# Kernel optimization log

Measured on AMD Instinct MI355X. Metric: run time of the kernel, lower is better.

## Reference

```python
import jax, jax.numpy as jnp
import numpy as np

B, S, H, I, E, K = 8, 4096, 512, 2048, 8, 2

def setup_inputs() -> dict:
    key = jax.random.key(0)
    ks = jax.random.split(key, 7)
    sH = 1.0 / np.sqrt(H)
    sI = 1.0 / np.sqrt(I)
    return {
        "x": jax.random.normal(ks[0], (B, S, H), dtype=jnp.float32),
        "gate_w": jax.random.uniform(ks[1], (H, E), jnp.float32, -sH, sH),
        "gate_b": jnp.zeros((E,), jnp.float32),
        "w1": jax.random.uniform(ks[2], (E, H, I), jnp.float32, -sH, sH),
        "b1": jax.random.uniform(ks[3], (E, I), jnp.float32, -sH, sH),
        "w2": jax.random.uniform(ks[4], (E, I, H), jnp.float32, -sI, sI),
        "b2": jax.random.uniform(ks[5], (E, H), jnp.float32, -sI, sI),
    }

def reference(x, gate_w, gate_b, w1, b1, w2, b2):
    # Gating: softmax over experts, top-k, renormalize selected probs via softmax.
    gate_probs = jax.nn.softmax(x @ gate_w + gate_b, axis=-1)          # [B,S,E]
    top_v, top_i = jax.lax.top_k(gate_probs, K)                        # [B,S,K]
    top_w = jax.nn.softmax(top_v, axis=-1)                             # renormalized
    out = jnp.zeros_like(x)
    for e in range(E):  # small fixed expert count
        # combine weight per token for expert e (0 if not routed here)
        ce = jnp.sum(jnp.where(top_i == e, top_w, 0.0), axis=-1)       # [B,S]
        h = jax.nn.relu(jnp.einsum("bsh,hi->bsi", x, w1[e]) + b1[e])   # [B,S,I]
        ye = jnp.einsum("bsi,ih->bsh", h, w2[e]) + b2[e]               # [B,S,H]
        out = out + ce[..., None] * ye
    return out
```

## Files before the change

### kernel.cpp

```cpp
#include <hip/hip_runtime.h>
#include <hip/hip_bf16.h>
#include <cstdint>

#define T_TOK 32768
#define HD 512
#define ID 2048
#define NE 8
#define ROWS_PAD_MAX 66560

typedef __bf16 bf16x8 __attribute__((ext_vector_type(8)));
typedef float f32x4 __attribute__((ext_vector_type(4)));

__device__ __forceinline__ ushort f2bf(float f) {
  __hip_bfloat16 h = __float2bfloat16(f);
  return *reinterpret_cast<ushort*>(&h);
}

__device__ __forceinline__ void gload16(const ushort* g, ushort* l) {
  __builtin_amdgcn_global_load_lds((__attribute__((address_space(1))) void*)(void*)g,
                                   (__attribute__((address_space(3))) void*)(void*)l,
                                   16, 0, 0);
}

__global__ void k_zero(float4* out4, int n4, int* counts) {
  if (blockIdx.x == 0 && threadIdx.x < NE) counts[threadIdx.x] = 0;
  float4 z = make_float4(0.f, 0.f, 0.f, 0.f);
  for (int i = blockIdx.x * blockDim.x + threadIdx.x; i < n4; i += gridDim.x * blockDim.x)
    out4[i] = z;
}

__global__ void k_transpose(const float* __restrict__ in, ushort* __restrict__ out, int R, int C) {
  __shared__ float tile[32][33];
  int z = blockIdx.z;
  const float* src = in + (size_t)z * R * C;
  ushort* dst = out + (size_t)z * R * C;
  int c0 = blockIdx.x * 32, r0 = blockIdx.y * 32;
  int tx = threadIdx.x, ty = threadIdx.y;
#pragma unroll
  for (int i = 0; i < 32; i += 8)
    tile[ty + i][tx] = src[(size_t)(r0 + ty + i) * C + c0 + tx];
  __syncthreads();
#pragma unroll
  for (int i = 0; i < 32; i += 8)
    dst[(size_t)(c0 + ty + i) * R + r0 + tx] = f2bf(tile[tx][ty + i]);
}

__global__ __launch_bounds__(256) void k_cast_gate(const float* __restrict__ x,
                                                   const float* __restrict__ gw,
                                                   const float* __restrict__ gb,
                                                   ushort* __restrict__ xb,
                                                   uchar2* __restrict__ tope,
                                                   float2* __restrict__ tw) {
  int t = blockIdx.x * 4 + (threadIdx.x >> 6);
  int lane = threadIdx.x & 63;
  const float4* xr = (const float4*)(x + (size_t)t * HD);
  float4 v0 = xr[lane];
  float4 v1 = xr[lane + 64];
  ushort4 o0, o1;
  o0.x = f2bf(v0.x); o0.y = f2bf(v0.y); o0.z = f2bf(v0.z); o0.w = f2bf(v0.w);
  o1.x = f2bf(v1.x); o1.y = f2bf(v1.y); o1.z = f2bf(v1.z); o1.w = f2bf(v1.w);
  ushort4* xw = (ushort4*)(xb + (size_t)t * HD);
  xw[lane] = o0;
  xw[lane + 64] = o1;
  float xv[8] = {v0.x, v0.y, v0.z, v0.w, v1.x, v1.y, v1.z, v1.w};
  float p[8] = {0, 0, 0, 0, 0, 0, 0, 0};
  const float* g0 = gw + (size_t)lane * 4 * 8;
  const float* g1 = gw + (size_t)(256 + lane * 4) * 8;
#pragma unroll
  for (int j = 0; j < 4; ++j)
#pragma unroll
    for (int e = 0; e < 8; ++e) p[e] += xv[j] * g0[j * 8 + e];
#pragma unroll
  for (int j = 0; j < 4; ++j)
#pragma unroll
    for (int e = 0; e < 8; ++e) p[e] += xv[4 + j] * g1[j * 8 + e];
#pragma unroll
  for (int e = 0; e < 8; ++e) {
    float s = p[e];
    for (int off = 32; off; off >>= 1) s += __shfl_xor(s, off);
    p[e] = s + gb[e];
  }
  float mx = p[0];
#pragma unroll
  for (int e = 1; e < 8; ++e) mx = fmaxf(mx, p[e]);
  float Z = 0.f;
  float pr[8];
#pragma unroll
  for (int e = 0; e < 8; ++e) { pr[e] = expf(p[e] - mx); Z += pr[e]; }
  float invZ = 1.f / Z;
#pragma unroll
  for (int e = 0; e < 8; ++e) pr[e] *= invZ;
  float v1v = pr[0]; int i1 = 0;
#pragma unroll
  for (int e = 1; e < 8; ++e) { if (pr[e] > v1v) { v1v = pr[e]; i1 = e; } }
  float v2v = -1.f; int i2 = 0;
#pragma unroll
  for (int e = 0; e < 8; ++e) { if (e != i1 && pr[e] > v2v) { v2v = pr[e]; i2 = e; } }
  float c1 = 1.f / (1.f + expf(v2v - v1v));
  float c2 = 1.f - c1;
  if (lane == 0) {
    tope[t] = make_uchar2((unsigned char)i1, (unsigned char)i2);
    tw[t] = make_float2(c1, c2);
  }
}

__global__ __launch_bounds__(256) void k_route(const uchar2* __restrict__ tope,
                                               const float2* __restrict__ tw,
                                               int* __restrict__ rtok, float* __restrict__ rw,
                                               int* __restrict__ counts) {
  int t = blockIdx.x * 256 + threadIdx.x;
  int lane = threadIdx.x & 63;
  uchar2 ei = tope[t];
  float2 c = tw[t];
  unsigned long long below = (1ull << lane) - 1ull;
#pragma unroll
  for (int e = 0; e < NE; ++e) {
    bool sel = (ei.x == e) || (ei.y == e);
    unsigned long long mask = __ballot(sel);
    if (mask == 0ull) continue;
    int cnt = __popcll(mask);
    int base = 0;
    if (lane == 0) base = atomicAdd(&counts[e], cnt);
    base = __shfl(base, 0);
    if (sel) {
      int pos = base + __popcll(mask & below);
      rtok[e * T_TOK + pos] = t;
      rw[e * T_TOK + pos] = (ei.x == e) ? c.x : c.y;
    }
  }
}

__global__ void k_offsets(const int* __restrict__ counts, int* __restrict__ poff) {
  if (threadIdx.x == 0) {
    int acc = 0;
    poff[0] = 0;
#pragma unroll
    for (int e = 0; e < NE; ++e) {
      acc += ((counts[e] + 127) >> 7) << 7;
      poff[e + 1] = acc;
    }
  }
}

__device__ __forceinline__ int find_expert(const int* poff, int v) {
  int e = 0;
#pragma unroll
  for (int j = 1; j < NE; ++j) e += (v >= poff[j]) ? 1 : 0;
  return e;
}

__global__ __launch_bounds__(256) void k_ffn1(const ushort* __restrict__ xb,
                                              const ushort* __restrict__ w1t,
                                              const float* __restrict__ b1,
                                              const int* __restrict__ rtok,
                                              const int* __restrict__ counts,
                                              const int* __restrict__ poff,
                                              ushort* __restrict__ h, int wb128) {
  int mb = wb128 + blockIdx.x;
  int v = mb << 7;
  if (v >= poff[NE]) return;
  int e = find_expert(poff, v);
  int cnt = counts[e];
  int m0 = v - poff[e];
  int n0 = blockIdx.y * 128;
  __shared__ __attribute__((aligned(16))) ushort As[128 * 32];
  __shared__ __attribute__((aligned(16))) ushort Bs[128 * 32];
  int tid = threadIdx.x, lane = tid & 63, wv = tid >> 6;
  int c0id = wv * 128 + lane, c1id = c0id + 64;
  int rA0 = c0id >> 2, rA1 = c1id >> 2;
  int kq0 = (c0id & 3) * 8, kq1 = (c1id & 3) * 8;
  const int* rte = rtok + e * T_TOK;
  int tok0 = rte[min(m0 + rA0, cnt - 1)];
  int tok1 = rte[min(m0 + rA1, cnt - 1)];
  const ushort* aSrc0 = xb + (size_t)tok0 * HD + kq0;
  const ushort* aSrc1 = xb + (size_t)tok1 * HD + kq1;
  const ushort* bBase = w1t + ((size_t)e * ID + n0) * HD;
  const ushort* bSrc0 = bBase + (size_t)rA0 * HD + kq0;
  const ushort* bSrc1 = bBase + (size_t)rA1 * HD + kq1;
  ushort* aDst = As + (size_t)wv * 128 * 8;
  ushort* bDst = Bs + (size_t)wv * 128 * 8;
  f32x4 acc[4][4] = {};
  int lr = lane & 15, lk = lane >> 4;
  int wr = wv >> 1, wc = wv & 1;
  const ushort* aRd = As + ((wr * 64 + lr) * 32 + lk * 8);
  const ushort* bRd = Bs + ((wc * 64 + lr) * 32 + lk * 8);
  for (int k0 = 0; k0 < HD; k0 += 32) {
    gload16(aSrc0 + k0, aDst);
    gload16(aSrc1 + k0, aDst + 64 * 8);
    gload16(bSrc0 + k0, bDst);
    gload16(bSrc1 + k0, bDst + 64 * 8);
    __syncthreads();
    bf16x8 af[4], bfr[4];
#pragma unroll
    for (int i = 0; i < 4; ++i) {
      af[i] = *(const bf16x8*)(aRd + i * 16 * 32);
      bfr[i] = *(const bf16x8*)(bRd + i * 16 * 32);
    }
#pragma unroll
    for (int mi = 0; mi < 4; ++mi)
#pragma unroll
      for (int ni = 0; ni < 4; ++ni)
        acc[mi][ni] = __builtin_amdgcn_mfma_f32_16x16x32_bf16(af[mi], bfr[ni], acc[mi][ni], 0, 0, 0);
    __syncthreads();
  }
  int hrow0 = blockIdx.x * 128;
#pragma unroll
  for (int ni = 0; ni < 4; ++ni) {
    int ng = n0 + wc * 64 + ni * 16 + lr;
    float bv = b1[e * ID + ng];
#pragma unroll
    for (int mi = 0; mi < 4; ++mi) {
      int rbase = hrow0 + wr * 64 + mi * 16 + lk * 4;
#pragma unroll
      for (int r = 0; r < 4; ++r) {
        float v2 = acc[mi][ni][r] + bv;
        v2 = fmaxf(v2, 0.f);
        h[(size_t)(rbase + r) * ID + ng] = f2bf(v2);
      }
    }
  }
}

__global__ __launch_bounds__(256) void k_ffn2(const ushort* __restrict__ h,
                                              const ushort* __restrict__ w2t,
                                              const float* __restrict__ b2,
                                              const int* __restrict__ rtok,
                                              const float* __restrict__ rw,
                                              const int* __restrict__ counts,
                                              const int* __restrict__ poff,
                                              float* __restrict__ out, int wb128) {
  int mb = wb128 + blockIdx.x;
  int v = mb << 7;
  if (v >= poff[NE]) return;
  int e = find_expert(poff, v);
  int cnt = counts[e];
  int m0 = v - poff[e];
  int n0 = blockIdx.y * 128;
  int ks = blockIdx.z;
  __shared__ __attribute__((aligned(16))) ushort As[128 * 32];
  __shared__ __attribute__((aligned(16))) ushort Bs[128 * 32];
  __shared__ int stok[128];
  __shared__ float scoef[128];
  int tid = threadIdx.x, lane = tid & 63, wv = tid >> 6;
  if (tid < 128) {
    int idx = min(m0 + tid, cnt - 1);
    stok[tid] = rtok[e * T_TOK + idx];
    scoef[tid] = rw[e * T_TOK + idx];
  }
  int c0id = wv * 128 + lane, c1id = c0id + 64;
  int rA0 = c0id >> 2, rA1 = c1id >> 2;
  int kq0 = (c0id & 3) * 8, kq1 = (c1id & 3) * 8;
  int hrow0 = blockIdx.x * 128;
  const ushort* aSrc0 = h + (size_t)(hrow0 + rA0) * ID + kq0;
  const ushort* aSrc1 = h + (size_t)(hrow0 + rA1) * ID + kq1;
  const ushort* bBase = w2t + ((size_t)e * HD + n0) * ID;
  const ushort* bSrc0 = bBase + (size_t)rA0 * ID + kq0;
  const ushort* bSrc1 = bBase + (size_t)rA1 * ID + kq1;
  ushort* aDst = As + (size_t)wv * 128 * 8;
  ushort* bDst = Bs + (size_t)wv * 128 * 8;
  f32x4 acc[4][4] = {};
  int lr = lane & 15, lk = lane >> 4;
  int wr = wv >> 1, wc = wv & 1;
  const ushort* aRd = As + ((wr * 64 + lr) * 32 + lk * 8);
  const ushort* bRd = Bs + ((wc * 64 + lr) * 32 + lk * 8);
  int kbeg = ks * (ID / 2), kend = kbeg + ID / 2;
  for (int k0 = kbeg; k0 < kend; k0 += 32) {
    gload16(aSrc0 + k0, aDst);
    gload16(aSrc1 + k0, aDst + 64 * 8);
    gload16(bSrc0 + k0, bDst);
    gload16(bSrc1 + k0, bDst + 64 * 8);
    __syncthreads();
    bf16x8 af[4], bfr[4];
#pragma unroll
    for (int i = 0; i < 4; ++i) {
      af[i] = *(const bf16x8*)(aRd + i * 16 * 32);
      bfr[i] = *(const bf16x8*)(bRd + i * 16 * 32);
    }
#pragma unroll
    for (int mi = 0; mi < 4; ++mi)
#pragma unroll
      for (int ni = 0; ni < 4; ++ni)
        acc[mi][ni] = __builtin_amdgcn_mfma_f32_16x16x32_bf16(af[mi], bfr[ni], acc[mi][ni], 0, 0, 0);
    __syncthreads();
  }
#pragma unroll
  for (int ni = 0; ni < 4; ++ni) {
    int ng = n0 + wc * 64 + ni * 16 + lr;
    float b2v = (ks == 0) ? b2[e * HD + ng] : 0.f;
#pragma unroll
    for (int mi = 0; mi < 4; ++mi) {
      int rloc = wr * 64 + mi * 16 + lk * 4;
#pragma unroll
      for (int r = 0; r < 4; ++r) {
        int m_l = rloc + r;
        if (m0 + m_l < cnt) {
          float vv = (acc[mi][ni][r] + b2v) * scoef[m_l];
          unsafeAtomicAdd(&out[(size_t)stok[m_l] * HD + ng], vv);
        }
      }
    }
  }
}

extern "C" void kernel_launch(void* const* d_in, const int* in_sizes, int n_in,
                              void* d_out, int out_size, void* d_ws, size_t ws_size,
                              hipStream_t stream) {
  const float* x  = (const float*)d_in[0];
  const float* gw = (const float*)d_in[1];
  const float* gb = (const float*)d_in[2];
  const float* w1 = (const float*)d_in[3];
  const float* b1 = (const float*)d_in[4];
  const float* w2 = (const float*)d_in[5];
  const float* b2 = (const float*)d_in[6];
  float* out = (float*)d_out;

  char* p = (char*)d_ws;
  ushort* xb   = (ushort*)p; p += (size_t)T_TOK * HD * 2;
  ushort* w1t  = (ushort*)p; p += (size_t)NE * ID * HD * 2;
  ushort* w2t  = (ushort*)p; p += (size_t)NE * HD * ID * 2;
  int*    rtok = (int*)p;    p += (size_t)NE * T_TOK * 4;
  float*  rw   = (float*)p;  p += (size_t)NE * T_TOK * 4;
  uchar2* tope = (uchar2*)p; p += (size_t)T_TOK * 2;
  float2* tw   = (float2*)p; p += (size_t)T_TOK * 8;
  int*  counts = (int*)p;
  int*  poff   = counts + 16;
  p += 128;
  ushort* hbuf = (ushort*)p;
  size_t fixed = (size_t)(p - (char*)d_ws);
  size_t avail = ws_size > fixed ? ws_size - fixed : 0;

  int Wmax = (int)((avail / ((size_t)ID * 2)) & ~(size_t)127);
  if (Wmax > ROWS_PAD_MAX) Wmax = ROWS_PAD_MAX;
  int W = (Wmax >= 16640) ? 16640 : Wmax;
  if (W < 128) W = 128;
  int nwin = (ROWS_PAD_MAX + W - 1) / W;
  int WB = W / 128;

  k_zero<<<2048, 256, 0, stream>>>((float4*)out, T_TOK * HD / 4, counts);
  k_cast_gate<<<T_TOK / 4, 256, 0, stream>>>(x, gw, gb, xb, tope, tw);
  k_route<<<T_TOK / 256, 256, 0, stream>>>(tope, tw, rtok, rw, counts);
  k_offsets<<<1, 64, 0, stream>>>(counts, poff);
  k_transpose<<<dim3(ID / 32, HD / 32, NE), dim3(32, 8), 0, stream>>>(w1, w1t, HD, ID);
  k_transpose<<<dim3(HD / 32, ID / 32, NE), dim3(32, 8), 0, stream>>>(w2, w2t, ID, HD);

  for (int w = 0; w < nwin; ++w) {
    int wb128 = w * WB;
    k_ffn1<<<dim3(WB, ID / 128), 256, 0, stream>>>(xb, w1t, b1, rtok, counts, poff, hbuf, wb128);
    k_ffn2<<<dim3(WB, HD / 128, 2), 256, 0, stream>>>(hbuf, w2t, b2, rtok, rw, counts, poff,
                                                      out, wb128);
  }
}
```

Measured before the change: 1.043 ms.

## Fuse both expert FFN GEMMs into one kernel keeping hidden chunks in LDS

Replaces the windowed pair of FFN1/FFN2 launches with a single fused kernel. Each 512-thread block owns a 128-row slab of routed tokens and computes the hidden activations 128 columns at a time into padded shared memory, then immediately accumulates them into the full 512-wide output with W2 fragments read straight from global memory. This removes the global hidden buffer round trip, the per-window launches and the split-K in FFN2. The cost is only 520 blocks with large per-thread accumulators, uncached W2 loads and FFN1 tiles that are now narrower.

New measurement: 1.353 ms. 29.7% more time.

```diff
diff --git a/kernel.cpp b/kernel.cpp
--- a/kernel.cpp
+++ b/kernel.cpp
@@ -7,6 +7,8 @@
 #define ID 2048
 #define NE 8
 #define ROWS_PAD_MAX 66560
+#define NMB 520
+#define HPAD 136
 
 typedef __bf16 bf16x8 __attribute__((ext_vector_type(8)));
 typedef float f32x4 __attribute__((ext_vector_type(4)));
@@ -149,153 +151,122 @@
   return e;
 }
 
-__global__ __launch_bounds__(256) void k_ffn1(const ushort* __restrict__ xb,
-                                              const ushort* __restrict__ w1t,
-                                              const float* __restrict__ b1,
-                                              const int* __restrict__ rtok,
-                                              const int* __restrict__ counts,
-                                              const int* __restrict__ poff,
-                                              ushort* __restrict__ h, int wb128) {
-  int mb = wb128 + blockIdx.x;
+__global__ __launch_bounds__(512, 2) void k_ffn(const ushort* __restrict__ xb,
+                                                const ushort* __restrict__ w1t,
+                                                const ushort* __restrict__ w2t,
+                                                const float* __restrict__ b1,
+                                                const float* __restrict__ b2,
+                                                const int* __restrict__ rtok,
+                                                const float* __restrict__ rw,
+                                                const int* __restrict__ counts,
+                                                const int* __restrict__ poff,
+                                                float* __restrict__ out) {
+  int bid = blockIdx.x;
+  int mb = (bid & 7) * (NMB / 8) + (bid >> 3);
   int v = mb << 7;
   if (v >= poff[NE]) return;
   int e = find_expert(poff, v);
   int cnt = counts[e];
   int m0 = v - poff[e];
-  int n0 = blockIdx.y * 128;
-  __shared__ __attribute__((aligned(16))) ushort As[128 * 32];
-  __shared__ __attribute__((aligned(16))) ushort Bs[128 * 32];
-  int tid = threadIdx.x, lane = tid & 63, wv = tid >> 6;
-  int c0id = wv * 128 + lane, c1id = c0id + 64;
-  int rA0 = c0id >> 2, rA1 = c1id >> 2;
-  int kq0 = (c0id & 3) * 8, kq1 = (c1id & 3) * 8;
-  const int* rte = rtok + e * T_TOK;
-  int tok0 = rte[min(m0 + rA0, cnt - 1)];
-  int tok1 = rte[min(m0 + rA1, cnt - 1)];
-  const ushort* aSrc0 = xb + (size_t)tok0 * HD + kq0;
-  const ushort* aSrc1 = xb + (size_t)tok1 * HD + kq1;
-  const ushort* bBase = w1t + ((size_t)e * ID + n0) * HD;
-  const ushort* bSrc0 = bBase + (size_t)rA0 * HD + kq0;
-  const ushort* bSrc1 = bBase + (size_t)rA1 * HD + kq1;
-  ushort* aDst = As + (size_t)wv * 128 * 8;
-  ushort* bDst = Bs + (size_t)wv * 128 * 8;
-  f32x4 acc[4][4] = {};
-  int lr = lane & 15, lk = lane >> 4;
-  int wr = wv >> 1, wc = wv & 1;
-  const ushort* aRd = As + ((wr * 64 + lr) * 32 + lk * 8);
-  const ushort* bRd = Bs + ((wc * 64 + lr) * 32 + lk * 8);
-  for (int k0 = 0; k0 < HD; k0 += 32) {
-    gload16(aSrc0 + k0, aDst);
-    gload16(aSrc1 + k0, aDst + 64 * 8);
-    gload16(bSrc0 + k0, bDst);
-    gload16(bSrc1 + k0, bDst + 64 * 8);
-    __syncthreads();
-    bf16x8 af[4], bfr[4];
-#pragma unroll
-    for (int i = 0; i < 4; ++i) {
-      af[i] = *(const bf16x8*)(aRd + i * 16 * 32);
-      bfr[i] = *(const bf16x8*)(bRd + i * 16 * 32);
-    }
-#pragma unroll
-    for (int mi = 0; mi < 4; ++mi)
-#pragma unroll
-      for (int ni = 0; ni < 4; ++ni)
-        acc[mi][ni] = __builtin_amdgcn_mfma_f32_16x16x32_bf16(af[mi], bfr[ni], acc[mi][ni], 0, 0, 0);
-    __syncthreads();
-  }
-  int hrow0 = blockIdx.x * 128;
-#pragma unroll
-  for (int ni = 0; ni < 4; ++ni) {
-    int ng = n0 + wc * 64 + ni * 16 + lr;
-    float bv = b1[e * ID + ng];
-#pragma unroll
-    for (int mi = 0; mi < 4; ++mi) {
-      int rbase = hrow0 + wr * 64 + mi * 16 + lk * 4;
-#pragma unroll
-      for (int r = 0; r < 4; ++r) {
-        float v2 = acc[mi][ni][r] + bv;
-        v2 = fmaxf(v2, 0.f);
-        h[(size_t)(rbase + r) * ID + ng] = f2bf(v2);
-      }
-    }
-  }
-}
-
-__global__ __launch_bounds__(256) void k_ffn2(const ushort* __restrict__ h,
-                                              const ushort* __restrict__ w2t,
-                                              const float* __restrict__ b2,
-                                              const int* __restrict__ rtok,
-                                              const float* __restrict__ rw,
-                                              const int* __restrict__ counts,
-                                              const int* __restrict__ poff,
-                                              float* __restrict__ out, int wb128) {
-  int mb = wb128 + blockIdx.x;
-  int v = mb << 7;
-  if (v >= poff[NE]) return;
-  int e = find_expert(poff, v);
-  int cnt = counts[e];
-  int m0 = v - poff[e];
-  int n0 = blockIdx.y * 128;
-  int ks = blockIdx.z;
-  __shared__ __attribute__((aligned(16))) ushort As[128 * 32];
-  __shared__ __attribute__((aligned(16))) ushort Bs[128 * 32];
+
+  __shared__ __attribute__((aligned(16))) ushort Xs[128 * 32];
+  __shared__ __attribute__((aligned(16))) ushort Ws[128 * 32];
+  __shared__ __attribute__((aligned(16))) ushort Hs[128 * HPAD];
   __shared__ int stok[128];
   __shared__ float scoef[128];
+
   int tid = threadIdx.x, lane = tid & 63, wv = tid >> 6;
+  int lr = lane & 15, lk = lane >> 4;
+  int wr = wv >> 2, wc = wv & 3;
+
   if (tid < 128) {
     int idx = min(m0 + tid, cnt - 1);
     stok[tid] = rtok[e * T_TOK + idx];
     scoef[tid] = rw[e * T_TOK + idx];
   }
-  int c0id = wv * 128 + lane, c1id = c0id + 64;
-  int rA0 = c0id >> 2, rA1 = c1id >> 2;
-  int kq0 = (c0id & 3) * 8, kq1 = (c1id & 3) * 8;
-  int hrow0 = blockIdx.x * 128;
-  const ushort* aSrc0 = h + (size_t)(hrow0 + rA0) * ID + kq0;
-  const ushort* aSrc1 = h + (size_t)(hrow0 + rA1) * ID + kq1;
-  const ushort* bBase = w2t + ((size_t)e * HD + n0) * ID;
-  const ushort* bSrc0 = bBase + (size_t)rA0 * ID + kq0;
-  const ushort* bSrc1 = bBase + (size_t)rA1 * ID + kq1;
-  ushort* aDst = As + (size_t)wv * 128 * 8;
-  ushort* bDst = Bs + (size_t)wv * 128 * 8;
-  f32x4 acc[4][4] = {};
-  int lr = lane & 15, lk = lane >> 4;
-  int wr = wv >> 1, wc = wv & 1;
-  const ushort* aRd = As + ((wr * 64 + lr) * 32 + lk * 8);
-  const ushort* bRd = Bs + ((wc * 64 + lr) * 32 + lk * 8);
-  int kbeg = ks * (ID / 2), kend = kbeg + ID / 2;
-  for (int k0 = kbeg; k0 < kend; k0 += 32) {
-    gload16(aSrc0 + k0, aDst);
-    gload16(aSrc1 + k0, aDst + 64 * 8);
-    gload16(bSrc0 + k0, bDst);
-    gload16(bSrc1 + k0, bDst + 64 * 8);
+  __syncthreads();
+
+  int srow = tid >> 2;
+  int skq = (tid & 3) * 8;
+  const ushort* aBase = xb + (size_t)stok[srow] * HD + skq;
+  const ushort* bBase0 = w1t + ((size_t)e * ID + srow) * HD + skq;
+  ushort* XsW = Xs + wv * 512;
+  ushort* WsW = Ws + wv * 512;
+
+  const ushort* w2b = w2t + ((size_t)e * HD + wc * 128 + lr) * ID + lk * 8;
+
+  f32x4 acc2[4][8] = {};
+
+#pragma unroll 1
+  for (int cc = 0; cc < ID / 128; ++cc) {
+    const ushort* bBase = bBase0 + (size_t)cc * 128 * HD;
+    float b1c0 = b1[e * ID + cc * 128 + wc * 32 + lr];
+    float b1c1 = b1[e * ID + cc * 128 + wc * 32 + 16 + lr];
+
+    f32x4 acc1[4][2] = {};
+    for (int k0 = 0; k0 < HD; k0 += 32) {
+      gload16(aBase + k0, XsW);
+      gload16(bBase + k0, WsW);
+      __syncthreads();
+      bf16x8 af[4], bfr[2];
+#pragma unroll
+      for (int i = 0; i < 4; ++i)
+        af[i] = *(const bf16x8*)(Xs + (wr * 64 + i * 16 + lr) * 32 + lk * 8);
+#pragma unroll
+      for (int i = 0; i < 2; ++i)
+        bfr[i] = *(const bf16x8*)(Ws + (wc * 32 + i * 16 + lr) * 32 + lk * 8);
+#pragma unroll
+      for (int mi = 0; mi < 4; ++mi)
+#pragma unroll
+        for (int ni = 0; ni < 2; ++ni)
+          acc1[mi][ni] = __builtin_amdgcn_mfma_f32_16x16x32_bf16(af[mi], bfr[ni], acc1[mi][ni], 0, 0, 0);
+      __syncthreads();
+    }
+
+#pragma unroll
+    for (int mi = 0; mi < 4; ++mi) {
+#pragma unroll
+      for (int ni = 0; ni < 2; ++ni) {
+        int icol = wc * 32 + ni * 16 + lr;
+        float bv = ni ? b1c1 : b1c0;
+#pragma unroll
+        for (int r = 0; r < 4; ++r) {
+          int m = wr * 64 + mi * 16 + lk * 4 + r;
+          Hs[m * HPAD + icol] = f2bf(fmaxf(acc1[mi][ni][r] + bv, 0.f));
+        }
+      }
+    }
     __syncthreads();
-    bf16x8 af[4], bfr[4];
-#pragma unroll
-    for (int i = 0; i < 4; ++i) {
-      af[i] = *(const bf16x8*)(aRd + i * 16 * 32);
-      bfr[i] = *(const bf16x8*)(bRd + i * 16 * 32);
-    }
-#pragma unroll
-    for (int mi = 0; mi < 4; ++mi)
-#pragma unroll
-      for (int ni = 0; ni < 4; ++ni)
-        acc[mi][ni] = __builtin_amdgcn_mfma_f32_16x16x32_bf16(af[mi], bfr[ni], acc[mi][ni], 0, 0, 0);
+
+#pragma unroll
+    for (int ks = 0; ks < 4; ++ks) {
+      bf16x8 a2[4];
+#pragma unroll
+      for (int mi = 0; mi < 4; ++mi)
+        a2[mi] = *(const bf16x8*)(Hs + (wr * 64 + mi * 16 + lr) * HPAD + ks * 32 + lk * 8);
+#pragma unroll
+      for (int ni = 0; ni < 8; ++ni) {
+        bf16x8 b2f = *(const bf16x8*)(w2b + (size_t)ni * 16 * ID + cc * 128 + ks * 32);
+#pragma unroll
+        for (int mi = 0; mi < 4; ++mi)
+          acc2[mi][ni] = __builtin_amdgcn_mfma_f32_16x16x32_bf16(a2[mi], b2f, acc2[mi][ni], 0, 0, 0);
+      }
+    }
     __syncthreads();
   }
-#pragma unroll
-  for (int ni = 0; ni < 4; ++ni) {
-    int ng = n0 + wc * 64 + ni * 16 + lr;
-    float b2v = (ks == 0) ? b2[e * HD + ng] : 0.f;
+
+#pragma unroll
+  for (int ni = 0; ni < 8; ++ni) {
+    int n = wc * 128 + ni * 16 + lr;
+    float b2v = b2[e * HD + n];
 #pragma unroll
     for (int mi = 0; mi < 4; ++mi) {
-      int rloc = wr * 64 + mi * 16 + lk * 4;
 #pragma unroll
       for (int r = 0; r < 4; ++r) {
-        int m_l = rloc + r;
-        if (m0 + m_l < cnt) {
-          float vv = (acc[mi][ni][r] + b2v) * scoef[m_l];
-          unsafeAtomicAdd(&out[(size_t)stok[m_l] * HD + ng], vv);
+        int m = wr * 64 + mi * 16 + lk * 4 + r;
+        if (m0 + m < cnt) {
+          float vv = (acc2[mi][ni][r] + b2v) * scoef[m];
+          unsafeAtomicAdd(&out[(size_t)stok[m] * HD + n], vv);
         }
       }
     }
@@ -325,16 +296,6 @@
   int*  counts = (int*)p;
   int*  poff   = counts + 16;
   p += 128;
-  ushort* hbuf = (ushort*)p;
-  size_t fixed = (size_t)(p - (char*)d_ws);
-  size_t avail = ws_size > fixed ? ws_size - fixed : 0;
-
-  int Wmax = (int)((avail / ((size_t)ID * 2)) & ~(size_t)127);
-  if (Wmax > ROWS_PAD_MAX) Wmax = ROWS_PAD_MAX;
-  int W = (Wmax >= 16640) ? 16640 : Wmax;
-  if (W < 128) W = 128;
-  int nwin = (ROWS_PAD_MAX + W - 1) / W;
-  int WB = W / 128;
 
   k_zero<<<2048, 256, 0, stream>>>((float4*)out, T_TOK * HD / 4, counts);
   k_cast_gate<<<T_TOK / 4, 256, 0, stream>>>(x, gw, gb, xb, tope, tw);
@@ -343,10 +304,5 @@
   k_transpose<<<dim3(ID / 32, HD / 32, NE), dim3(32, 8), 0, stream>>>(w1, w1t, HD, ID);
   k_transpose<<<dim3(HD / 32, ID / 32, NE), dim3(32, 8), 0, stream>>>(w2, w2t, ID, HD);
 
-  for (int w = 0; w < nwin; ++w) {
-    int wb128 = w * WB;
-    k_ffn1<<<dim3(WB, ID / 128), 256, 0, stream>>>(xb, w1t, b1, rtok, counts, poff, hbuf, wb128);
-    k_ffn2<<<dim3(WB, HD / 128, 2), 256, 0, stream>>>(hbuf, w2t, b2, rtok, rw, counts, poff,
-                                                      out, wb128);
-  }
-}
+  k_ffn<<<NMB, 512, 0, stream>>>(xb, w1t, w2t, b1, b2, rtok, rw, counts, poff, out);
+}
```
